# Kernel optimization log

Hardware: AMD Instinct MI355X
Metric: run time of the kernel (lower is better)

## Reference

```python
import jax, jax.numpy as jnp
import numpy as np

D_MODEL = 1024
NUM_HEADS = 16
HEAD_DIM = D_MODEL // NUM_HEADS


def setup_inputs() -> dict:
    key = jax.random.key(0)
    ks = jax.random.split(key, 6)
    B, S = 2, 2048
    s = 1.0 / np.sqrt(D_MODEL)
    return {
        "x": jax.random.normal(ks[0], (B, S, D_MODEL), dtype=jnp.float32),
        "Wq": jax.random.normal(ks[1], (D_MODEL, D_MODEL), dtype=jnp.float32) * s,
        "Wk": jax.random.normal(ks[2], (D_MODEL, D_MODEL), dtype=jnp.float32) * s,
        "Wv": jax.random.normal(ks[3], (D_MODEL, D_MODEL), dtype=jnp.float32) * s,
        "Wo": jax.random.normal(ks[4], (D_MODEL, D_MODEL), dtype=jnp.float32) * s,
        "bo": jax.random.normal(ks[5], (D_MODEL,), dtype=jnp.float32) * 0.01,
    }


def reference(x, Wq, Wk, Wv, Wo, bo):
    b, n, _ = x.shape
    # QKV projections (no bias, qkv_bias=False); weights applied as x @ W^T like nn.Linear
    q = (x @ Wq.T).reshape(b, n, NUM_HEADS, HEAD_DIM).transpose(0, 2, 1, 3)  # [b,h,n,d]
    k = (x @ Wk.T).reshape(b, n, NUM_HEADS, HEAD_DIM).transpose(0, 2, 1, 3)
    v = (x @ Wv.T).reshape(b, n, NUM_HEADS, HEAD_DIM).transpose(0, 2, 1, 3)
    scores = jnp.einsum("bhqd,bhkd->bhqk", q, k)
    causal = jnp.tril(jnp.ones((n, n), dtype=bool))  # keep where True
    scores = jnp.where(causal, scores, -jnp.inf)
    weights = jax.nn.softmax(scores / np.sqrt(HEAD_DIM), axis=-1)
    # dropout p=0.0 -> identity (eval semantics)
    ctx = jnp.einsum("bhqk,bhkd->bhqd", weights, v)
    ctx = ctx.transpose(0, 2, 1, 3).reshape(b, n, D_MODEL)
    return ctx @ Wo.T + bo
```

## Files before the change

kernel.cpp:

```cpp
#include <hip/hip_runtime.h>

#define D_MODEL 1024
#define NUM_HEADS 16
#define HEAD_DIM 64
#define BATCH 2
#define SEQ 2048
#define MTOT (BATCH * SEQ)

typedef __attribute__((ext_vector_type(8))) short bf16x8;
typedef __attribute__((ext_vector_type(4))) short s16x4;
typedef __attribute__((ext_vector_type(4))) float f32x4;
typedef unsigned short u16;
typedef unsigned long long u64;

__device__ __forceinline__ u16 f2bf(float f) {
    unsigned u = __float_as_uint(f);
    return (u16)((u + 0x7FFFu + ((u >> 16) & 1u)) >> 16);
}
__device__ __forceinline__ float bf2f(u16 v) {
    return __uint_as_float((unsigned)v << 16);
}

__device__ __forceinline__ unsigned cvt_pk_bf16(float lo, float hi) {
    unsigned r;
    asm volatile("v_cvt_pk_bf16_f32 %0, %1, %2" : "=v"(r) : "v"(lo), "v"(hi));
    return r;
}

#if __has_builtin(__builtin_amdgcn_exp2f)
#define EXP2(x) __builtin_amdgcn_exp2f(x)
#else
#define EXP2(x) exp2f(x)
#endif

#define GLOAD16(gp, lp) __builtin_amdgcn_global_load_lds(                      \
    (const __attribute__((address_space(1))) void*)(gp),                       \
    (__attribute__((address_space(3))) void*)(lp), 16, 0, 0)

__global__ __launch_bounds__(256)
void cast_all_kernel(const float* __restrict__ x,  const float* __restrict__ Wq,
                     const float* __restrict__ Wk, const float* __restrict__ Wv,
                     const float* __restrict__ Wo, u16* __restrict__ dst)
{
    const int i = blockIdx.x * 256 + threadIdx.x;
    const float* src;
    int j;
    if (i < 524288) { src = x; j = i; }
    else if (i < 917504) {
        const int k = i - 524288;
        const int z = k >> 17;
        src = (z == 0) ? Wq : (z == 1) ? Wk : Wv;
        j = k & 0x1FFFF;
    } else { src = Wo; j = i - 917504; }
    const float4* s = reinterpret_cast<const float4*>(src) + (size_t)j * 2;
    float4 a = s[0], b = s[1];
    u16 tmp[8] = {f2bf(a.x), f2bf(a.y), f2bf(a.z), f2bf(a.w),
                  f2bf(b.x), f2bf(b.y), f2bf(b.z), f2bf(b.w)};
    *reinterpret_cast<int4*>(dst + (size_t)i * 8) = *reinterpret_cast<int4*>(tmp);
}

__global__ __launch_bounds__(512, 6)
void gemm_qkv_kernel(const u16* __restrict__ A, const u16* __restrict__ B,
                     u16* __restrict__ Qo, u16* __restrict__ Ko, u16* __restrict__ Vt)
{
    __shared__ u16 Al[3][128 * 32];
    __shared__ u16 Bl[3][128 * 32];

    const int tid = threadIdx.x;
    const int l = tid & 63;
    const int w = tid >> 6;
    const int wm = w >> 2, wn = w & 3;
    const int lr = l & 15, lg = l >> 4;

    const int bid = blockIdx.x;
    const int swz = (bid & 7) * 96 + (bid >> 3);
    const int mb = swz / 24, nbv = swz % 24;
    const int m0 = mb * 128, n0 = nbv * 128;

    const int arow = tid >> 2;
    const int acol = ((tid & 3) ^ ((arow >> 1) & 3)) * 8;
    const int dstq = tid * 8;
    const int rsw  = (lr >> 1) & 3;

    f32x4 acc[4][2];
    #pragma unroll
    for (int i = 0; i < 4; ++i)
        #pragma unroll
        for (int j = 0; j < 2; ++j) acc[i][j] = (f32x4){0.f, 0.f, 0.f, 0.f};

    #pragma unroll
    for (int t = 0; t < 2; ++t) {
        const int k0 = t * 32;
        GLOAD16(A + (size_t)(m0 + arow) * D_MODEL + k0 + acol, &Al[t][dstq]);
        GLOAD16(B + (size_t)(n0 + arow) * D_MODEL + k0 + acol, &Bl[t][dstq]);
    }

    int cb = 0;
    for (int t = 0; t < 32; ++t) {
        if (t < 31) asm volatile("s_waitcnt vmcnt(2)" ::: "memory");
        else        asm volatile("s_waitcnt vmcnt(0)" ::: "memory");
        __builtin_amdgcn_s_barrier();

        if (t + 2 < 32) {
            const int sb = (cb >= 1) ? cb - 1 : cb + 2;
            const int k0 = (t + 2) * 32;
            GLOAD16(A + (size_t)(m0 + arow) * D_MODEL + k0 + acol, &Al[sb][dstq]);
            GLOAD16(B + (size_t)(n0 + arow) * D_MODEL + k0 + acol, &Bl[sb][dstq]);
        }

        const u16* __restrict__ Ab = Al[cb];
        const u16* __restrict__ Bb = Bl[cb];
        bf16x8 af[4], bfr[2];
        #pragma unroll
        for (int i = 0; i < 4; ++i)
            af[i] = *reinterpret_cast<const bf16x8*>(
                &Ab[(wm * 64 + i * 16 + lr) * 32 + ((lg ^ rsw) * 8)]);
        #pragma unroll
        for (int j = 0; j < 2; ++j)
            bfr[j] = *reinterpret_cast<const bf16x8*>(
                &Bb[(wn * 32 + j * 16 + lr) * 32 + ((lg ^ rsw) * 8)]);

        __builtin_amdgcn_s_setprio(1);
        #pragma unroll
        for (int i = 0; i < 4; ++i)
            #pragma unroll
            for (int j = 0; j < 2; ++j)
                acc[i][j] = __builtin_amdgcn_mfma_f32_16x16x32_bf16(
                    af[i], bfr[j], acc[i][j], 0, 0, 0);
        __builtin_amdgcn_s_setprio(0);

        cb = (cb == 2) ? 0 : cb + 1;
    }

    const int z = (n0 >> 10);
    if (z < 2) {
        #pragma unroll
        for (int i = 0; i < 4; ++i) {
            #pragma unroll
            for (int r = 0; r < 4; ++r) {
                const int m = m0 + wm * 64 + i * 16 + lg * 4 + r;
                const int bb = m >> 11, s = m & (SEQ - 1);
                #pragma unroll
                for (int j = 0; j < 2; ++j) {
                    const int c = n0 + wn * 32 + j * 16 + lr;
                    const int cc = c & 1023, h = cc >> 6, d = cc & 63;
                    const size_t idx = ((size_t)(bb * NUM_HEADS + h) * SEQ + s) * 64 + d;
                    if (z == 0) Qo[idx] = f2bf(acc[i][j][r] * 0.18033688f);
                    else        Ko[idx] = f2bf(acc[i][j][r]);
                }
            }
        }
    } else {
        #pragma unroll
        for (int i = 0; i < 4; ++i) {
            const int mbase = m0 + wm * 64 + i * 16 + lg * 4;
            const int bb = mbase >> 11, s = mbase & (SEQ - 1);
            #pragma unroll
            for (int j = 0; j < 2; ++j) {
                const int c = n0 + wn * 32 + j * 16 + lr;
                const int cc = c & 1023, h = cc >> 6, d = cc & 63;
                u16 t4[4];
                #pragma unroll
                for (int r = 0; r < 4; ++r) t4[r] = f2bf(acc[i][j][r]);
                *reinterpret_cast<u64*>(
                    &Vt[((size_t)(bb * NUM_HEADS + h) * 64 + d) * SEQ + s]) =
                    *reinterpret_cast<u64*>(t4);
            }
        }
    }
}

__global__ __launch_bounds__(512, 2)
void gemm_out_kernel(const u16* __restrict__ A, const u16* __restrict__ B,
                     const float* __restrict__ bias, float* __restrict__ out)
{
    __shared__ u16 Al[3][128 * 32];
    __shared__ u16 Bl[3][128 * 32];

    const int tid = threadIdx.x;
    const int l = tid & 63;
    const int w = tid >> 6;
    const int wm = w >> 2, wn = w & 3;
    const int lr = l & 15, lg = l >> 4;

    const int bid = blockIdx.x;
    const int swz = (bid & 7) * 32 + (bid >> 3);
    const int mb = swz >> 3, nb = swz & 7;
    const int m0 = mb * 128, n0 = nb * 128;

    const int arow = tid >> 2;
    const int acol = ((tid & 3) ^ ((arow >> 1) & 3)) * 8;
    const int dstq = tid * 8;
    const int rsw  = (lr >> 1) & 3;

    f32x4 acc[4][2];
    #pragma unroll
    for (int i = 0; i < 4; ++i)
        #pragma unroll
        for (int j = 0; j < 2; ++j) acc[i][j] = (f32x4){0.f, 0.f, 0.f, 0.f};

    #pragma unroll
    for (int t = 0; t < 2; ++t) {
        const int k0 = t * 32;
        GLOAD16(A + (size_t)(m0 + arow) * D_MODEL + k0 + acol, &Al[t][dstq]);
        GLOAD16(B + (size_t)(n0 + arow) * D_MODEL + k0 + acol, &Bl[t][dstq]);
    }

    int cb = 0;
    for (int t = 0; t < 32; ++t) {
        if (t < 31) asm volatile("s_waitcnt vmcnt(2)" ::: "memory");
        else        asm volatile("s_waitcnt vmcnt(0)" ::: "memory");
        __builtin_amdgcn_s_barrier();

        if (t + 2 < 32) {
            const int sb = (cb >= 1) ? cb - 1 : cb + 2;
            const int k0 = (t + 2) * 32;
            GLOAD16(A + (size_t)(m0 + arow) * D_MODEL + k0 + acol, &Al[sb][dstq]);
            GLOAD16(B + (size_t)(n0 + arow) * D_MODEL + k0 + acol, &Bl[sb][dstq]);
        }

        const u16* __restrict__ Ab = Al[cb];
        const u16* __restrict__ Bb = Bl[cb];
        bf16x8 af[4], bfr[2];
        #pragma unroll
        for (int i = 0; i < 4; ++i)
            af[i] = *reinterpret_cast<const bf16x8*>(
                &Ab[(wm * 64 + i * 16 + lr) * 32 + ((lg ^ rsw) * 8)]);
        #pragma unroll
        for (int j = 0; j < 2; ++j)
            bfr[j] = *reinterpret_cast<const bf16x8*>(
                &Bb[(wn * 32 + j * 16 + lr) * 32 + ((lg ^ rsw) * 8)]);

        __builtin_amdgcn_s_setprio(1);
        #pragma unroll
        for (int i = 0; i < 4; ++i)
            #pragma unroll
            for (int j = 0; j < 2; ++j)
                acc[i][j] = __builtin_amdgcn_mfma_f32_16x16x32_bf16(
                    af[i], bfr[j], acc[i][j], 0, 0, 0);
        __builtin_amdgcn_s_setprio(0);

        cb = (cb == 2) ? 0 : cb + 1;
    }

    #pragma unroll
    for (int i = 0; i < 4; ++i) {
        #pragma unroll
        for (int r = 0; r < 4; ++r) {
            const int m = m0 + wm * 64 + i * 16 + lg * 4 + r;
            #pragma unroll
            for (int j = 0; j < 2; ++j) {
                const int c = n0 + wn * 32 + j * 16 + lr;
                out[(size_t)m * D_MODEL + c] = acc[i][j][r] + bias[c];
            }
        }
    }
}

__device__ __forceinline__ void map_pair128(int p, int& qt2, int& ch) {
    if (p < 16)      { qt2 = 15 - (p >> 2); ch = p & 3; }
    else if (p < 28) { int t = p - 16; qt2 = 11 - t / 3; ch = t % 3; }
    else if (p < 36) { int t = p - 28; qt2 = 7 - (t >> 1); ch = t & 1; }
    else             { qt2 = 39 - p; ch = 0; }
}

__global__ __launch_bounds__(256)
void attn_kernel(const u16* __restrict__ Q, const u16* __restrict__ K,
                 const u16* __restrict__ Vt, u16* __restrict__ ctx,
                 u16* __restrict__ Opart, float* __restrict__ Lpart)
{
    __shared__ char LdsB[2][16384];

    const int tid = threadIdx.x;
    const int l = tid & 63;
    const int w = tid >> 6;
    const int lr = l & 15;
    const int lg = l >> 4;

    const int xcd  = blockIdx.x & 7;
    const int slot = blockIdx.x >> 3;
    const int bh   = xcd * 4 + slot / 40;
    int qt2, ch;
    map_pair128(slot % 40, qt2, ch);

    const int ntiles = 2 * qt2 + 2;
    const int nch  = (ntiles + 7) >> 3;
    const int base = ntiles / nch, rem = ntiles % nch;
    const int start = ch * base + (ch < rem ? ch : rem);
    const int cnt   = base + (ch < rem ? 1 : 0);

    const size_t hbase = (size_t)bh * SEQ * 64;
    const int b = bh >> 4, h = bh & (NUM_HEADS - 1);
    const u16* __restrict__ Kh = K + hbase;
    const u16* __restrict__ Vh = Vt + hbase;
    const int q0 = qt2 * 128;

    const int r0 = tid >> 3;
    const int c0 = ((tid & 7) ^ (r0 & 7)) * 8;
    const int r1 = (256 + tid) >> 3;
    const int c1 = ((tid & 7) ^ (r1 & 7)) * 8;
    const int d0b = tid * 16;
    const int d1b = 4096 + tid * 16;
    const int rswz = (lr & 7) << 4;

    bf16x8 qf[2][2];
    #pragma unroll
    for (int fq = 0; fq < 2; ++fq) {
        const u16* qp = Q + hbase + (size_t)(q0 + fq * 64 + w * 16 + lr) * 64 + lg * 8;
        qf[fq][0] = *reinterpret_cast<const bf16x8*>(qp);
        qf[fq][1] = *reinterpret_cast<const bf16x8*>(qp + 32);
    }
    asm volatile("s_waitcnt vmcnt(0)" ::: "memory");

    f32x4 acc[2][4];
    #pragma unroll
    for (int fq = 0; fq < 2; ++fq)
        #pragma unroll
        for (int nb = 0; nb < 4; ++nb) acc[fq][nb] = (f32x4){0.f, 0.f, 0.f, 0.f};
    float lsumv[2] = {0.f, 0.f};

    {
        char* kb = LdsB[0];
        char* vb = LdsB[0] + 8192;
        const int kb64 = start * 64;
        GLOAD16(Kh + (size_t)(kb64 + r0) * 64 + c0, kb + d0b);
        GLOAD16(Kh + (size_t)(kb64 + r1) * 64 + c1, kb + d1b);
        GLOAD16(Vh + (size_t)r0 * SEQ + kb64 + c0, vb + d0b);
        GLOAD16(Vh + (size_t)r1 * SEQ + kb64 + c1, vb + d1b);
    }

    for (int it = 0; it < cnt; ++it) {
        const int tile = start + it;
        const int buf = it & 1;

        asm volatile("s_waitcnt vmcnt(0)" ::: "memory");
        __builtin_amdgcn_s_barrier();

        if (it < cnt - 1) {
            const int kb64 = (tile + 1) * 64;
            char* kbl = LdsB[buf ^ 1];
            char* vbl = kbl + 8192;
            GLOAD16(Kh + (size_t)(kb64 + r0) * 64 + c0, kbl + d0b);
            GLOAD16(Kh + (size_t)(kb64 + r1) * 64 + c1, kbl + d1b);
            GLOAD16(Vh + (size_t)r0 * SEQ + kb64 + c0, vbl + d0b);
            GLOAD16(Vh + (size_t)r1 * SEQ + kb64 + c1, vbl + d1b);
        }

        const char* kbuf = LdsB[buf];
        const char* vbuf = kbuf + 8192;

        bf16x8 kf[4][2];
        #pragma unroll
        for (int m = 0; m < 4; ++m) {
            const char* krow = kbuf + (16 * m + lr) * 128;
            kf[m][0] = *reinterpret_cast<const bf16x8*>(krow + ((lg * 16) ^ rswz));
            kf[m][1] = *reinterpret_cast<const bf16x8*>(krow + ((64 + lg * 16) ^ rswz));
        }

        const bool diag = (tile >= 2 * qt2);
        const int koff0 = (tile - 2 * qt2) * 64;

        unsigned dw[2][4][2];
        __builtin_amdgcn_s_setprio(1);
        #pragma unroll
        for (int fq = 0; fq < 2; ++fq) {
            f32x4 s[4];
            #pragma unroll
            for (int m = 0; m < 4; ++m) {
                s[m] = (f32x4){0.f, 0.f, 0.f, 0.f};
                s[m] = __builtin_amdgcn_mfma_f32_16x16x32_bf16(kf[m][0], qf[fq][0], s[m], 0, 0, 0);
                s[m] = __builtin_amdgcn_mfma_f32_16x16x32_bf16(kf[m][1], qf[fq][1], s[m], 0, 0, 0);
            }
            if (diag) {
                const int qloc = fq * 64 + w * 16 + lr;
                #pragma unroll
                for (int m = 0; m < 4; ++m)
                    #pragma unroll
                    for (int r = 0; r < 4; ++r)
                        if (koff0 + 16 * m + 4 * lg + r > qloc) s[m][r] = -1.0e38f;
            }
            float p[4][4];
            #pragma unroll
            for (int m = 0; m < 4; ++m) {
                #pragma unroll
                for (int r = 0; r < 4; ++r) p[m][r] = EXP2(s[m][r]);
                lsumv[fq] += (p[m][0] + p[m][1]) + (p[m][2] + p[m][3]);
                dw[fq][m][0] = cvt_pk_bf16(p[m][0], p[m][1]);
                dw[fq][m][1] = cvt_pk_bf16(p[m][2], p[m][3]);
            }
        }

        #pragma unroll
        for (int c = 0; c < 2; ++c) {
            union Pu { unsigned u[4]; bf16x8 v; } pb[2];
            #pragma unroll
            for (int fq = 0; fq < 2; ++fq) {
                pb[fq].u[0] = dw[fq][2 * c][0];     pb[fq].u[1] = dw[fq][2 * c][1];
                pb[fq].u[2] = dw[fq][2 * c + 1][0]; pb[fq].u[3] = dw[fq][2 * c + 1][1];
            }
            #pragma unroll
            for (int nb = 0; nb < 4; ++nb) {
                const char* vrow = vbuf + (16 * nb + lr) * 128;
                union Vu { s16x4 hv[2]; bf16x8 v; } vf;
                vf.hv[0] = *reinterpret_cast<const s16x4*>(
                    vrow + ((c * 64 + lg * 8) ^ rswz));
                vf.hv[1] = *reinterpret_cast<const s16x4*>(
                    vrow + ((c * 64 + 32 + lg * 8) ^ rswz));
                acc[0][nb] = __builtin_amdgcn_mfma_f32_16x16x32_bf16(
                    vf.v, pb[0].v, acc[0][nb], 0, 0, 0);
                acc[1][nb] = __builtin_amdgcn_mfma_f32_16x16x32_bf16(
                    vf.v, pb[1].v, acc[1][nb], 0, 0, 0);
            }
        }
        __builtin_amdgcn_s_setprio(0);
    }

    #pragma unroll
    for (int fq = 0; fq < 2; ++fq) {
        lsumv[fq] += __shfl_xor(lsumv[fq], 16);
        lsumv[fq] += __shfl_xor(lsumv[fq], 32);
    }

    if (nch == 1) {
        #pragma unroll
        for (int fq = 0; fq < 2; ++fq) {
            const float inv = 1.0f / lsumv[fq];
            const int qrow = q0 + fq * 64 + w * 16 + lr;
            u16* op = ctx + ((size_t)(b * SEQ) + qrow) * D_MODEL + h * 64 + 4 * lg;
            #pragma unroll
            for (int nb = 0; nb < 4; ++nb) {
                u16 t4[4];
                #pragma unroll
                for (int r = 0; r < 4; ++r) t4[r] = f2bf(acc[fq][nb][r] * inv);
                *reinterpret_cast<u64*>(op + 16 * nb) = *reinterpret_cast<u64*>(t4);
            }
        }
    } else {
        const int slot4 = ((bh * 12 + (qt2 - 4)) << 2) + ch;
        #pragma unroll
        for (int fq = 0; fq < 2; ++fq) {
            const int rloc = fq * 64 + w * 16 + lr;
            u16* op = Opart + (size_t)slot4 * 8192 + rloc * 64 + 4 * lg;
            #pragma unroll
            for (int nb = 0; nb < 4; ++nb) {
                u16 t4[4];
                #pragma unroll
                for (int r = 0; r < 4; ++r) t4[r] = f2bf(acc[fq][nb][r]);
                *reinterpret_cast<u64*>(op + 16 * nb) = *reinterpret_cast<u64*>(t4);
            }
            if (lg == 0) Lpart[slot4 * 128 + rloc] = lsumv[fq];
        }
    }
}

__global__ __launch_bounds__(128)
void attn_reduce_kernel(const u16* __restrict__ Opart,
                        const float* __restrict__ Lpart,
                        u16* __restrict__ ctx)
{
    const int blk = blockIdx.x;
    const int bh = blk / 12, idx = blk % 12;
    const int qt2 = idx + 4;
    const int nch = (2 * qt2 + 2 + 7) >> 3;
    const int t = threadIdx.x;
    const int b = bh >> 4, h = bh & (NUM_HEADS - 1);
    const int slot0 = (bh * 12 + idx) << 2;

    float acc[64] = {};
    float lt = 0.f;
    for (int ch = 0; ch < nch; ++ch) {
        const u16* op = Opart + (size_t)(slot0 + ch) * 8192 + t * 64;
        lt += Lpart[(slot0 + ch) * 128 + t];
        #pragma unroll
        for (int cchunk = 0; cchunk < 8; ++cchunk) {
            u16 v[8];
            *reinterpret_cast<int4*>(v) =
                *reinterpret_cast<const int4*>(op + cchunk * 8);
            #pragma unroll
            for (int j = 0; j < 8; ++j) acc[cchunk * 8 + j] += bf2f(v[j]);
        }
    }
    const float inv = 1.0f / lt;
    u16* orow = ctx + ((size_t)(b * SEQ) + qt2 * 128 + t) * D_MODEL + h * 64;
    #pragma unroll
    for (int cchunk = 0; cchunk < 8; ++cchunk) {
        u16 v[8];
        #pragma unroll
        for (int j = 0; j < 8; ++j) v[j] = f2bf(acc[cchunk * 8 + j] * inv);
        *reinterpret_cast<int4*>(orow + cchunk * 8) = *reinterpret_cast<int4*>(v);
    }
}


extern "C" void kernel_launch(void* const* d_in, const int* in_sizes, int n_in,
                              void* d_out, int out_size, void* d_ws, size_t ws_size,
                              hipStream_t stream)
{
    const float* x  = (const float*)d_in[0];
    const float* Wq = (const float*)d_in[1];
    const float* Wk = (const float*)d_in[2];
    const float* Wv = (const float*)d_in[3];
    const float* Wo = (const float*)d_in[4];
    const float* bo = (const float*)d_in[5];
    float* out = (float*)d_out;

    u16* xb   = (u16*)d_ws;
    u16* wqkv = xb   + (size_t)MTOT * D_MODEL;
    u16* wob  = wqkv + (size_t)3 * D_MODEL * D_MODEL;
    u16* Qw   = wob  + (size_t)D_MODEL * D_MODEL;
    u16* Kw   = Qw   + (size_t)MTOT * D_MODEL;
    u16* Vtw  = Kw   + (size_t)MTOT * D_MODEL;
    u16* ctxb = Vtw  + (size_t)MTOT * D_MODEL;
    u16* Opart = ctxb + (size_t)MTOT * D_MODEL;
    float* Lpart = (float*)(Opart + (size_t)1536 * 8192);

    cast_all_kernel<<<4096, 256, 0, stream>>>(x, Wq, Wk, Wv, Wo, xb);

    gemm_qkv_kernel<<<dim3(768), 512, 0, stream>>>(xb, wqkv, Qw, Kw, Vtw);

    attn_kernel<<<dim3(1280), 256, 0, stream>>>(Qw, Kw, Vtw, ctxb, Opart, Lpart);
    attn_reduce_kernel<<<dim3(384), 128, 0, stream>>>(Opart, Lpart, ctxb);

    gemm_out_kernel<<<dim3(256), 512, 0, stream>>>(ctxb, wob, bo, out);
}
```

Before: 111.5 us.

## Give each wave its own 32-row query tile, reading K/V directly from global

The attention work split changes from one 128-row query tile per block to an independent 32-row query tile per wave. This also changes the causal chunking and the split-K partial layout, and the reduce kernel now uses one thread per 8-column group. The LDS double buffering, barriers and async global-to-LDS loads are removed, so each wave reads K and V fragments straight from global memory. This removes block-level synchronisation and tail imbalance, and launch bounds are set to allow more occupancy. In exchange, K/V reuse across the four waves now relies on the cache, and loads are no longer prefetched.

```diff
diff --git a/kernel.cpp b/kernel.cpp
--- a/kernel.cpp
+++ b/kernel.cpp
@@ -257,35 +257,31 @@
     }
 }
 
-__device__ __forceinline__ void map_pair128(int p, int& qt2, int& ch) {
-    if (p < 16)      { qt2 = 15 - (p >> 2); ch = p & 3; }
-    else if (p < 28) { int t = p - 16; qt2 = 11 - t / 3; ch = t % 3; }
-    else if (p < 36) { int t = p - 28; qt2 = 7 - (t >> 1); ch = t & 1; }
-    else             { qt2 = 39 - p; ch = 0; }
-}
-
-__global__ __launch_bounds__(256)
+__global__ __launch_bounds__(256, 3)
 void attn_kernel(const u16* __restrict__ Q, const u16* __restrict__ K,
                  const u16* __restrict__ Vt, u16* __restrict__ ctx,
                  u16* __restrict__ Opart, float* __restrict__ Lpart)
 {
-    __shared__ char LdsB[2][16384];
-
     const int tid = threadIdx.x;
     const int l = tid & 63;
-    const int w = tid >> 6;
+    const int wv = tid >> 6;
     const int lr = l & 15;
     const int lg = l >> 4;
 
     const int xcd  = blockIdx.x & 7;
     const int slot = blockIdx.x >> 3;
     const int bh   = xcd * 4 + slot / 40;
-    int qt2, ch;
-    map_pair128(slot % 40, qt2, ch);
-
-    const int ntiles = 2 * qt2 + 2;
-    const int nch  = (ntiles + 7) >> 3;
-    const int base = ntiles / nch, rem = ntiles % nch;
+    const int p    = (slot % 40) * 4 + wv;
+
+    int t, ch;
+    if (p < 64)       { t = 63 - (p >> 2); ch = p & 3; }
+    else if (p < 112) { int q = p - 64;  t = 47 - q / 3;    ch = q % 3; }
+    else if (p < 144) { int q = p - 112; t = 31 - (q >> 1); ch = q & 1; }
+    else              { t = 159 - p; ch = 0; }
+
+    const int nt  = (t + 2) >> 1;
+    const int nch = (nt + 7) >> 3;
+    const int base = nt / nch, rem = nt % nch;
     const int start = ch * base + (ch < rem ? ch : rem);
     const int cnt   = base + (ch < rem ? 1 : 0);
 
@@ -293,24 +289,15 @@
     const int b = bh >> 4, h = bh & (NUM_HEADS - 1);
     const u16* __restrict__ Kh = K + hbase;
     const u16* __restrict__ Vh = Vt + hbase;
-    const int q0 = qt2 * 128;
-
-    const int r0 = tid >> 3;
-    const int c0 = ((tid & 7) ^ (r0 & 7)) * 8;
-    const int r1 = (256 + tid) >> 3;
-    const int c1 = ((tid & 7) ^ (r1 & 7)) * 8;
-    const int d0b = tid * 16;
-    const int d1b = 4096 + tid * 16;
-    const int rswz = (lr & 7) << 4;
+    const int q0 = t * 32;
 
     bf16x8 qf[2][2];
     #pragma unroll
     for (int fq = 0; fq < 2; ++fq) {
-        const u16* qp = Q + hbase + (size_t)(q0 + fq * 64 + w * 16 + lr) * 64 + lg * 8;
+        const u16* qp = Q + hbase + (size_t)(q0 + fq * 16 + lr) * 64 + lg * 8;
         qf[fq][0] = *reinterpret_cast<const bf16x8*>(qp);
         qf[fq][1] = *reinterpret_cast<const bf16x8*>(qp + 32);
     }
-    asm volatile("s_waitcnt vmcnt(0)" ::: "memory");
 
     f32x4 acc[2][4];
     #pragma unroll
@@ -319,49 +306,19 @@
         for (int nb = 0; nb < 4; ++nb) acc[fq][nb] = (f32x4){0.f, 0.f, 0.f, 0.f};
     float lsumv[2] = {0.f, 0.f};
 
-    {
-        char* kb = LdsB[0];
-        char* vb = LdsB[0] + 8192;
-        const int kb64 = start * 64;
-        GLOAD16(Kh + (size_t)(kb64 + r0) * 64 + c0, kb + d0b);
-        GLOAD16(Kh + (size_t)(kb64 + r1) * 64 + c1, kb + d1b);
-        GLOAD16(Vh + (size_t)r0 * SEQ + kb64 + c0, vb + d0b);
-        GLOAD16(Vh + (size_t)r1 * SEQ + kb64 + c1, vb + d1b);
-    }
-
     for (int it = 0; it < cnt; ++it) {
-        const int tile = start + it;
-        const int buf = it & 1;
-
-        asm volatile("s_waitcnt vmcnt(0)" ::: "memory");
-        __builtin_amdgcn_s_barrier();
-
-        if (it < cnt - 1) {
-            const int kb64 = (tile + 1) * 64;
-            char* kbl = LdsB[buf ^ 1];
-            char* vbl = kbl + 8192;
-            GLOAD16(Kh + (size_t)(kb64 + r0) * 64 + c0, kbl + d0b);
-            GLOAD16(Kh + (size_t)(kb64 + r1) * 64 + c1, kbl + d1b);
-            GLOAD16(Vh + (size_t)r0 * SEQ + kb64 + c0, vbl + d0b);
-            GLOAD16(Vh + (size_t)r1 * SEQ + kb64 + c1, vbl + d1b);
-        }
-
-        const char* kbuf = LdsB[buf];
-        const char* vbuf = kbuf + 8192;
+        const int T = start + it;
+        const u16* __restrict__ kb = Kh + (size_t)T * 64 * 64;
 
         bf16x8 kf[4][2];
         #pragma unroll
         for (int m = 0; m < 4; ++m) {
-            const char* krow = kbuf + (16 * m + lr) * 128;
-            kf[m][0] = *reinterpret_cast<const bf16x8*>(krow + ((lg * 16) ^ rswz));
-            kf[m][1] = *reinterpret_cast<const bf16x8*>(krow + ((64 + lg * 16) ^ rswz));
-        }
-
-        const bool diag = (tile >= 2 * qt2);
-        const int koff0 = (tile - 2 * qt2) * 64;
+            const u16* kr = kb + (size_t)(16 * m + lr) * 64 + lg * 8;
+            kf[m][0] = *reinterpret_cast<const bf16x8*>(kr);
+            kf[m][1] = *reinterpret_cast<const bf16x8*>(kr + 32);
+        }
 
         unsigned dw[2][4][2];
-        __builtin_amdgcn_s_setprio(1);
         #pragma unroll
         for (int fq = 0; fq < 2; ++fq) {
             f32x4 s[4];
@@ -371,22 +328,22 @@
                 s[m] = __builtin_amdgcn_mfma_f32_16x16x32_bf16(kf[m][0], qf[fq][0], s[m], 0, 0, 0);
                 s[m] = __builtin_amdgcn_mfma_f32_16x16x32_bf16(kf[m][1], qf[fq][1], s[m], 0, 0, 0);
             }
-            if (diag) {
-                const int qloc = fq * 64 + w * 16 + lr;
+            if (T == nt - 1) {
+                const int qg = q0 + fq * 16 + lr;
                 #pragma unroll
                 for (int m = 0; m < 4; ++m)
                     #pragma unroll
                     for (int r = 0; r < 4; ++r)
-                        if (koff0 + 16 * m + 4 * lg + r > qloc) s[m][r] = -1.0e38f;
-            }
-            float p[4][4];
+                        if (T * 64 + 16 * m + 4 * lg + r > qg) s[m][r] = -1.0e38f;
+            }
+            float pv[4][4];
             #pragma unroll
             for (int m = 0; m < 4; ++m) {
                 #pragma unroll
-                for (int r = 0; r < 4; ++r) p[m][r] = EXP2(s[m][r]);
-                lsumv[fq] += (p[m][0] + p[m][1]) + (p[m][2] + p[m][3]);
-                dw[fq][m][0] = cvt_pk_bf16(p[m][0], p[m][1]);
-                dw[fq][m][1] = cvt_pk_bf16(p[m][2], p[m][3]);
+                for (int r = 0; r < 4; ++r) pv[m][r] = EXP2(s[m][r]);
+                lsumv[fq] += (pv[m][0] + pv[m][1]) + (pv[m][2] + pv[m][3]);
+                dw[fq][m][0] = cvt_pk_bf16(pv[m][0], pv[m][1]);
+                dw[fq][m][1] = cvt_pk_bf16(pv[m][2], pv[m][3]);
             }
         }
 
@@ -400,19 +357,16 @@
             }
             #pragma unroll
             for (int nb = 0; nb < 4; ++nb) {
-                const char* vrow = vbuf + (16 * nb + lr) * 128;
+                const u16* vr = Vh + (size_t)(16 * nb + lr) * SEQ + T * 64 + c * 32 + lg * 4;
                 union Vu { s16x4 hv[2]; bf16x8 v; } vf;
-                vf.hv[0] = *reinterpret_cast<const s16x4*>(
-                    vrow + ((c * 64 + lg * 8) ^ rswz));
-                vf.hv[1] = *reinterpret_cast<const s16x4*>(
-                    vrow + ((c * 64 + 32 + lg * 8) ^ rswz));
+                vf.hv[0] = *reinterpret_cast<const s16x4*>(vr);
+                vf.hv[1] = *reinterpret_cast<const s16x4*>(vr + 16);
                 acc[0][nb] = __builtin_amdgcn_mfma_f32_16x16x32_bf16(
                     vf.v, pb[0].v, acc[0][nb], 0, 0, 0);
                 acc[1][nb] = __builtin_amdgcn_mfma_f32_16x16x32_bf16(
                     vf.v, pb[1].v, acc[1][nb], 0, 0, 0);
             }
         }
-        __builtin_amdgcn_s_setprio(0);
     }
 
     #pragma unroll
@@ -425,7 +379,7 @@
         #pragma unroll
         for (int fq = 0; fq < 2; ++fq) {
             const float inv = 1.0f / lsumv[fq];
-            const int qrow = q0 + fq * 64 + w * 16 + lr;
+            const int qrow = q0 + fq * 16 + lr;
             u16* op = ctx + ((size_t)(b * SEQ) + qrow) * D_MODEL + h * 64 + 4 * lg;
             #pragma unroll
             for (int nb = 0; nb < 4; ++nb) {
@@ -436,11 +390,11 @@
             }
         }
     } else {
-        const int slot4 = ((bh * 12 + (qt2 - 4)) << 2) + ch;
+        const int slot4 = (bh * 48 + (t - 16)) * 4 + ch;
         #pragma unroll
         for (int fq = 0; fq < 2; ++fq) {
-            const int rloc = fq * 64 + w * 16 + lr;
-            u16* op = Opart + (size_t)slot4 * 8192 + rloc * 64 + 4 * lg;
+            const int rloc = fq * 16 + lr;
+            u16* op = Opart + (size_t)slot4 * 2048 + rloc * 64 + 4 * lg;
             #pragma unroll
             for (int nb = 0; nb < 4; ++nb) {
                 u16 t4[4];
@@ -448,47 +402,42 @@
                 for (int r = 0; r < 4; ++r) t4[r] = f2bf(acc[fq][nb][r]);
                 *reinterpret_cast<u64*>(op + 16 * nb) = *reinterpret_cast<u64*>(t4);
             }
-            if (lg == 0) Lpart[slot4 * 128 + rloc] = lsumv[fq];
-        }
-    }
-}
-
-__global__ __launch_bounds__(128)
+            if (lg == 0) Lpart[slot4 * 32 + rloc] = lsumv[fq];
+        }
+    }
+}
+
+__global__ __launch_bounds__(256)
 void attn_reduce_kernel(const u16* __restrict__ Opart,
                         const float* __restrict__ Lpart,
                         u16* __restrict__ ctx)
 {
     const int blk = blockIdx.x;
-    const int bh = blk / 12, idx = blk % 12;
-    const int qt2 = idx + 4;
-    const int nch = (2 * qt2 + 2 + 7) >> 3;
-    const int t = threadIdx.x;
+    const int bh = blk / 48, t16 = blk % 48;
+    const int t = t16 + 16;
+    const int nt = (t + 2) >> 1;
+    const int nch = (nt + 7) >> 3;
+    const int row = threadIdx.x >> 3;
+    const int cg  = threadIdx.x & 7;
     const int b = bh >> 4, h = bh & (NUM_HEADS - 1);
-    const int slot0 = (bh * 12 + idx) << 2;
-
-    float acc[64] = {};
+    const int slot0 = (bh * 48 + t16) * 4;
+
+    float acc[8] = {};
     float lt = 0.f;
     for (int ch = 0; ch < nch; ++ch) {
-        const u16* op = Opart + (size_t)(slot0 + ch) * 8192 + t * 64;
-        lt += Lpart[(slot0 + ch) * 128 + t];
-        #pragma unroll
-        for (int cchunk = 0; cchunk < 8; ++cchunk) {
-            u16 v[8];
-            *reinterpret_cast<int4*>(v) =
-                *reinterpret_cast<const int4*>(op + cchunk * 8);
-            #pragma unroll
-            for (int j = 0; j < 8; ++j) acc[cchunk * 8 + j] += bf2f(v[j]);
-        }
+        const u16* op = Opart + (size_t)(slot0 + ch) * 2048 + row * 64 + cg * 8;
+        lt += Lpart[(slot0 + ch) * 32 + row];
+        u16 v[8];
+        *reinterpret_cast<int4*>(v) = *reinterpret_cast<const int4*>(op);
+        #pragma unroll
+        for (int j = 0; j < 8; ++j) acc[j] += bf2f(v[j]);
     }
     const float inv = 1.0f / lt;
-    u16* orow = ctx + ((size_t)(b * SEQ) + qt2 * 128 + t) * D_MODEL + h * 64;
-    #pragma unroll
-    for (int cchunk = 0; cchunk < 8; ++cchunk) {
-        u16 v[8];
-        #pragma unroll
-        for (int j = 0; j < 8; ++j) v[j] = f2bf(acc[cchunk * 8 + j] * inv);
-        *reinterpret_cast<int4*>(orow + cchunk * 8) = *reinterpret_cast<int4*>(v);
-    }
+    u16 v[8];
+    #pragma unroll
+    for (int j = 0; j < 8; ++j) v[j] = f2bf(acc[j] * inv);
+    u16* orow = ctx + ((size_t)(b * SEQ) + t * 32 + row) * D_MODEL + h * 64 + cg * 8;
+    *reinterpret_cast<int4*>(orow) = *reinterpret_cast<int4*>(v);
 }
 
 
@@ -512,14 +461,14 @@
     u16* Vtw  = Kw   + (size_t)MTOT * D_MODEL;
     u16* ctxb = Vtw  + (size_t)MTOT * D_MODEL;
     u16* Opart = ctxb + (size_t)MTOT * D_MODEL;
-    float* Lpart = (float*)(Opart + (size_t)1536 * 8192);
+    float* Lpart = (float*)(Opart + (size_t)6144 * 2048);
 
     cast_all_kernel<<<4096, 256, 0, stream>>>(x, Wq, Wk, Wv, Wo, xb);
 
     gemm_qkv_kernel<<<dim3(768), 512, 0, stream>>>(xb, wqkv, Qw, Kw, Vtw);
 
     attn_kernel<<<dim3(1280), 256, 0, stream>>>(Qw, Kw, Vtw, ctxb, Opart, Lpart);
-    attn_reduce_kernel<<<dim3(384), 128, 0, stream>>>(Opart, Lpart, ctxb);
+    attn_reduce_kernel<<<dim3(1536), 256, 0, stream>>>(Opart, Lpart, ctxb);
 
     gemm_out_kernel<<<dim3(256), 512, 0, stream>>>(ctxb, wob, bo, out);
 }
```

New measurement: 188.8 us. 1.69x slower.
